# Kernel tuning notes

Hardware: AMD Instinct MI355X
Metric: run time of the kernel (lower is better)

The kernel has to match this reference:

```python
import jax, jax.numpy as jnp
import numpy as np

N_SPARSE, N_SEQ, N_DENSE = 16, 2, 13
VOCAB, EMBED_DIM, SEQ_LEN = 100000, 64, 50
BATCH = 4096


def setup_inputs() -> dict:
    key = jax.random.key(0)
    k1, k2, k3, k4, k5 = jax.random.split(key, 5)
    return {
        "sparse_tables": jax.random.normal(k1, (N_SPARSE, VOCAB, EMBED_DIM), dtype=jnp.float32),
        "seq_tables": jax.random.normal(k2, (N_SEQ, VOCAB, EMBED_DIM), dtype=jnp.float32),
        "dense_vals": jax.random.normal(k3, (BATCH, N_DENSE), dtype=jnp.float32),
        "sparse_idx": jax.random.randint(k4, (N_SPARSE, BATCH), 0, VOCAB, dtype=jnp.int32),
        "seq_idx": jax.random.randint(k5, (N_SEQ, BATCH, SEQ_LEN), 0, VOCAB, dtype=jnp.int32),
    }


def reference(sparse_tables, seq_tables, dense_vals, sparse_idx, seq_idx):
    # Per-feature gather for sparse features: [F, B, D] -> [B, F, D]
    sparse_emb = jax.vmap(lambda tab, idx: tab[idx])(sparse_tables, sparse_idx)
    sparse_emb = jnp.transpose(sparse_emb, (1, 0, 2))  # [B, N_SPARSE, D]

    # Sequence feature gathers: [N_SEQ, B, S, D]
    seq_emb = jax.vmap(lambda tab, idx: tab[idx])(seq_tables, seq_idx)

    # Feature 0: SumPooling -> [B, D]
    sum_pooled = jnp.sum(seq_emb[0], axis=1)

    # Feature 1: AveragePooling (divide per embed-dim by count of nonzero
    # embedding values along seq, exactly as the torch module does)
    e = seq_emb[1]  # [B, S, D]
    non_padding = jnp.sum((e != 0).astype(jnp.float32), axis=1)  # [B, D]
    mean_pooled = jnp.sum(e, axis=1) / (non_padding + 1e-16)

    # Concat along feature axis then flatten (squeeze_dim=True path)
    all_emb = jnp.concatenate(
        [sparse_emb, sum_pooled[:, None, :], mean_pooled[:, None, :]], axis=1
    )  # [B, N_SPARSE + N_SEQ, D]
    flat = all_emb.reshape(all_emb.shape[0], -1)
    return jnp.concatenate([flat, dense_vals], axis=1)  # [B, 18*64 + 13]
```

## Files before the change

### kernel.cpp

```cpp
#include <hip/hip_runtime.h>

#define N_SPARSE 16
#define N_SEQ    2
#define N_DENSE  13
#define VOCAB    100000
#define EMBED    64
#define SEQ_LEN  50
#define BATCH    4096
#define N_FEAT   (N_SPARSE + N_SEQ)
#define OUT_COLS (N_FEAT * EMBED + N_DENSE)

#define EMB_TASKS   (BATCH * N_FEAT)
#define EMB_BLOCKS  (EMB_TASKS / 4)
#define DENSE_ELEMS (BATCH * N_DENSE)
#define DENSE_BLOCKS ((DENSE_ELEMS + 255) / 256)

__global__ __launch_bounds__(256) void emb_kernel(
    const float* __restrict__ sparse_tables,
    const float* __restrict__ seq_tables,
    const float* __restrict__ dense_vals,
    const int* __restrict__ sparse_idx,
    const int* __restrict__ seq_idx,
    float* __restrict__ out)
{
    int blk = blockIdx.x;

    if (blk < EMB_BLOCKS) {
        int task = blk * 4 + (threadIdx.x >> 6);
        int lane = threadIdx.x & 63;
        int fidx = task >> 12;
        int b    = task & (BATCH - 1);
        if (fidx >= N_SEQ) {
            int f   = fidx - N_SEQ;
            int idx = sparse_idx[f * BATCH + b];
            float v = sparse_tables[((size_t)(f * VOCAB + idx)) * EMBED + lane];
            out[(size_t)b * OUT_COLS + f * EMBED + lane] = v;
        } else {
            int sf = fidx;
            const int* ip = seq_idx + ((size_t)(sf * BATCH + b)) * SEQ_LEN;
            int myidx = (lane < SEQ_LEN) ? ip[lane] : 0;
            const float* tab = seq_tables + (size_t)sf * VOCAB * EMBED;

            float acc = 0.f;
            float cnt = 0.f;
            #pragma unroll
            for (int s = 0; s < SEQ_LEN; ++s) {
                int idx = __shfl(myidx, s);
                float fv = tab[(size_t)idx * EMBED + lane];
                acc += fv;
                cnt += (fv != 0.f) ? 1.f : 0.f;
            }
            float r = (sf == 0) ? acc : acc / (cnt + 1e-16f);
            out[(size_t)b * OUT_COLS + (N_SPARSE + sf) * EMBED + lane] = r;
        }
    } else {
        int e = (blk - EMB_BLOCKS) * 256 + threadIdx.x;
        if (e < DENSE_ELEMS) {
            int b = e / N_DENSE;
            int j = e - b * N_DENSE;
            out[(size_t)b * OUT_COLS + N_FEAT * EMBED + j] = dense_vals[e];
        }
    }
}

extern "C" void kernel_launch(void* const* d_in, const int* in_sizes, int n_in,
                              void* d_out, int out_size, void* d_ws, size_t ws_size,
                              hipStream_t stream) {
    const float* sparse_tables = (const float*)d_in[0];
    const float* seq_tables    = (const float*)d_in[1];
    const float* dense_vals    = (const float*)d_in[2];
    const int*   sparse_idx    = (const int*)d_in[3];
    const int*   seq_idx       = (const int*)d_in[4];
    float*       out           = (float*)d_out;

    dim3 grid(EMB_BLOCKS + DENSE_BLOCKS);
    dim3 block(256);
    emb_kernel<<<grid, block, 0, stream>>>(sparse_tables, seq_tables, dense_vals,
                                           sparse_idx, seq_idx, out);
}
```

Baseline: 490.0 us.

## Use float4 gathers with 4 rows per wave and merge sparse rows per batch

The sequence pooling now loads four embedding rows per wave instruction as float4 vectors, with 16 lanes per row, and combines the partial sums across the four row groups with xor shuffles. Each sparse wave now handles all 16 sparse features plus the dense values for one batch row, instead of launching separate per-feature waves and dense blocks. The aim is fewer load instructions, more memory-level parallelism per wave, and a smaller grid. The cost is extra cross-lane reduction and stores that are not coalesced as well, since each lane writes four scalars.

```diff
diff --git a/kernel.cpp b/kernel.cpp
--- a/kernel.cpp
+++ b/kernel.cpp
@@ -10,10 +10,10 @@
 #define N_FEAT   (N_SPARSE + N_SEQ)
 #define OUT_COLS (N_FEAT * EMBED + N_DENSE)
 
-#define EMB_TASKS   (BATCH * N_FEAT)
-#define EMB_BLOCKS  (EMB_TASKS / 4)
-#define DENSE_ELEMS (BATCH * N_DENSE)
-#define DENSE_BLOCKS ((DENSE_ELEMS + 255) / 256)
+#define SEQ_WAVES (N_SEQ * BATCH)
+#define SB_WAVES  (BATCH)
+#define TOT_WAVES (SEQ_WAVES + SB_WAVES)
+#define NBLOCKS   (TOT_WAVES / 4)
 
 __global__ __launch_bounds__(256) void emb_kernel(
     const float* __restrict__ sparse_tables,
@@ -23,43 +23,87 @@
     const int* __restrict__ seq_idx,
     float* __restrict__ out)
 {
-    int blk = blockIdx.x;
+    const int w    = blockIdx.x * 4 + (threadIdx.x >> 6);
+    const int lane = threadIdx.x & 63;
+    const int g    = lane >> 4;
+    const int l16  = lane & 15;
 
-    if (blk < EMB_BLOCKS) {
-        int task = blk * 4 + (threadIdx.x >> 6);
-        int lane = threadIdx.x & 63;
-        int fidx = task >> 12;
-        int b    = task & (BATCH - 1);
-        if (fidx >= N_SEQ) {
-            int f   = fidx - N_SEQ;
-            int idx = sparse_idx[f * BATCH + b];
-            float v = sparse_tables[((size_t)(f * VOCAB + idx)) * EMBED + lane];
-            out[(size_t)b * OUT_COLS + f * EMBED + lane] = v;
-        } else {
-            int sf = fidx;
-            const int* ip = seq_idx + ((size_t)(sf * BATCH + b)) * SEQ_LEN;
-            int myidx = (lane < SEQ_LEN) ? ip[lane] : 0;
-            const float* tab = seq_tables + (size_t)sf * VOCAB * EMBED;
+    if (w < SEQ_WAVES) {
+        const int sf = w >> 12;
+        const int b  = w & (BATCH - 1);
+        const int* ip = seq_idx + ((size_t)(sf * BATCH + b)) * SEQ_LEN;
+        int myidx = (lane < SEQ_LEN) ? ip[lane] : 0;
+        const float* tab = seq_tables + (size_t)sf * VOCAB * EMBED;
 
-            float acc = 0.f;
-            float cnt = 0.f;
-            #pragma unroll
-            for (int s = 0; s < SEQ_LEN; ++s) {
-                int idx = __shfl(myidx, s);
-                float fv = tab[(size_t)idx * EMBED + lane];
-                acc += fv;
-                cnt += (fv != 0.f) ? 1.f : 0.f;
+        float ax = 0.f, ay = 0.f, az = 0.f, aw = 0.f;
+        float cx = 0.f, cy = 0.f, cz = 0.f, cw = 0.f;
+
+        #pragma unroll
+        for (int i = 0; i < 12; ++i) {
+            const int row = i * 4 + g;
+            const int idx = __shfl(myidx, row);
+            const float4 v = *reinterpret_cast<const float4*>(
+                tab + (size_t)idx * EMBED + 4 * l16);
+            ax += v.x; ay += v.y; az += v.z; aw += v.w;
+            cx += (v.x != 0.f) ? 1.f : 0.f;
+            cy += (v.y != 0.f) ? 1.f : 0.f;
+            cz += (v.z != 0.f) ? 1.f : 0.f;
+            cw += (v.w != 0.f) ? 1.f : 0.f;
+        }
+        {
+            const int row = 48 + g;
+            const int idx = __shfl(myidx, (row < SEQ_LEN) ? row : 0);
+            if (row < SEQ_LEN) {
+                const float4 v = *reinterpret_cast<const float4*>(
+                    tab + (size_t)idx * EMBED + 4 * l16);
+                ax += v.x; ay += v.y; az += v.z; aw += v.w;
+                cx += (v.x != 0.f) ? 1.f : 0.f;
+                cy += (v.y != 0.f) ? 1.f : 0.f;
+                cz += (v.z != 0.f) ? 1.f : 0.f;
+                cw += (v.w != 0.f) ? 1.f : 0.f;
             }
-            float r = (sf == 0) ? acc : acc / (cnt + 1e-16f);
-            out[(size_t)b * OUT_COLS + (N_SPARSE + sf) * EMBED + lane] = r;
+        }
+
+        ax += __shfl_xor(ax, 16); ax += __shfl_xor(ax, 32);
+        ay += __shfl_xor(ay, 16); ay += __shfl_xor(ay, 32);
+        az += __shfl_xor(az, 16); az += __shfl_xor(az, 32);
+        aw += __shfl_xor(aw, 16); aw += __shfl_xor(aw, 32);
+        if (sf == 1) {
+            cx += __shfl_xor(cx, 16); cx += __shfl_xor(cx, 32);
+            cy += __shfl_xor(cy, 16); cy += __shfl_xor(cy, 32);
+            cz += __shfl_xor(cz, 16); cz += __shfl_xor(cz, 32);
+            cw += __shfl_xor(cw, 16); cw += __shfl_xor(cw, 32);
+            ax = ax / (cx + 1e-16f);
+            ay = ay / (cy + 1e-16f);
+            az = az / (cz + 1e-16f);
+            aw = aw / (cw + 1e-16f);
+        }
+
+        if (lane < 16) {
+            float* o = out + (size_t)b * OUT_COLS + (N_SPARSE + sf) * EMBED + 4 * l16;
+            o[0] = ax; o[1] = ay; o[2] = az; o[3] = aw;
         }
     } else {
-        int e = (blk - EMB_BLOCKS) * 256 + threadIdx.x;
-        if (e < DENSE_ELEMS) {
-            int b = e / N_DENSE;
-            int j = e - b * N_DENSE;
-            out[(size_t)b * OUT_COLS + N_FEAT * EMBED + j] = dense_vals[e];
+        const int b = w - SEQ_WAVES;
+        int myidx16 = (lane < N_SPARSE) ? sparse_idx[lane * BATCH + b] : 0;
+
+        float4 v[4];
+        #pragma unroll
+        for (int i = 0; i < 4; ++i) {
+            const int f   = i * 4 + g;
+            const int idx = __shfl(myidx16, f);
+            v[i] = *reinterpret_cast<const float4*>(
+                sparse_tables + ((size_t)f * VOCAB + idx) * EMBED + 4 * l16);
         }
+        float* ob = out + (size_t)b * OUT_COLS;
+        #pragma unroll
+        for (int i = 0; i < 4; ++i) {
+            const int f = i * 4 + g;
+            float* o = ob + f * EMBED + 4 * l16;
+            o[0] = v[i].x; o[1] = v[i].y; o[2] = v[i].z; o[3] = v[i].w;
+        }
+        if (lane < N_DENSE)
+            ob[N_FEAT * EMBED + lane] = dense_vals[b * N_DENSE + lane];
     }
 }
 
@@ -73,8 +117,6 @@
     const int*   seq_idx       = (const int*)d_in[4];
     float*       out           = (float*)d_out;
 
-    dim3 grid(EMB_BLOCKS + DENSE_BLOCKS);
-    dim3 block(256);
-    emb_kernel<<<grid, block, 0, stream>>>(sparse_tables, seq_tables, dense_vals,
-                                           sparse_idx, seq_idx, out);
+    emb_kernel<<<dim3(NBLOCKS), dim3(256), 0, stream>>>(
+        sparse_tables, seq_tables, dense_vals, sparse_idx, seq_idx, out);
 }
```

Measured after the change: 481.8 us. No clear change (-1.7%).
